# Optimization experiments

Hardware: AMD Instinct MI355X
Metric: run time of the kernel (lower is better)

The kernel has to match this reference:

```python
import jax, jax.numpy as jnp
import numpy as np

BS, M, D_IN, D_OUT = 32, 128, 64, 32


def _spd_log(X):
    # torch.svd on an SPD matrix == eigh (u diag(s) u^T with s>0), so
    # u @ diag(log s) @ v^T reduces to u @ diag(log s) @ u^T.
    s, u = jnp.linalg.eigh(X)
    return jnp.einsum('...ik,...k,...jk->...ij', u, jnp.log(s), u)


def _sym_exp(X):
    s, u = jnp.linalg.eigh(X)
    return jnp.einsum('...ik,...k,...jk->...ij', u, jnp.exp(s), u)


def setup_inputs() -> dict:
    key = jax.random.key(0)
    kx, kq, kk, kv = jax.random.split(key, 4)
    A = jax.random.normal(kx, (BS, M, D_IN, D_IN), dtype=jnp.float32)
    # SPD input: A A^T / d_in + eps I (eigenvalues strictly positive)
    x = jnp.einsum('bmij,bmkj->bmik', A, A) / D_IN + 1e-2 * jnp.eye(D_IN, dtype=jnp.float32)
    def stiefel(k):
        # column-orthonormal (d_in, d_out), mimicking SPDTransform's Stiefel weight
        return jnp.linalg.qr(jax.random.normal(k, (D_IN, D_OUT), dtype=jnp.float32))[0]
    return {'x': x, 'Wq': stiefel(kq), 'Wk': stiefel(kk), 'Wv': stiefel(kv)}


def reference(x, Wq, Wk, Wv):
    bs, m, d_in, _ = x.shape
    d_out = Wq.shape[1]

    def bimap(W):  # SPDTransform: W^T X W, stays SPD
        return jnp.einsum('pi,bmpq,qj->bmij', W, x, W)

    Q, K, V = bimap(Wq), bimap(Wk), bimap(Wv)
    logQ, logK, logV = _spd_log(Q), _spd_log(K), _spd_log(V)

    # log-Euclidean distance: sum of singular values of D D^T with
    # D = log A - log B (symmetric) equals trace(D D^T) = ||D||_F^2.
    # Torch's repeat/expand pattern yields energy[b,i,j] = d(K_i, Q_j);
    # computed here without materializing the (bs, m, m, d, d) tensor.
    q2 = jnp.sum(logQ * logQ, axis=(-2, -1))            # [bs, m]
    k2 = jnp.sum(logK * logK, axis=(-2, -1))            # [bs, m]
    cross = jnp.einsum('bikl,bjkl->bij', logK, logQ)    # [bs, m(i=K), m(j=Q)]
    energy = k2[:, :, None] + q2[:, None, :] - 2.0 * cross

    scores = 1.0 / (1.0 + jnp.log1p(energy))
    # softmax over dim=-2 (the K index i), then permute(0, 2, 1)
    attn = jnp.swapaxes(jax.nn.softmax(scores, axis=-2), -1, -2)  # [bs, j, i]

    # LogEuclideanMean: exp_sym( sum_i attn[b,j,i] * log V[b,i] )
    mean_log = jnp.einsum('bji,bikl->bjkl', attn, logV)
    out = _sym_exp(mean_log)
    return out.reshape(bs * m, d_out, d_out)
```

## Files before the change

### kernel.cpp

```cpp
#include <hip/hip_runtime.h>
#include <math.h>

constexpr int kBS = 32, kM = 128, kNMAT = kBS * kM;
constexpr int kDIN = 64, kDOUT = 32, kMSZ = kDOUT * kDOUT;
constexpr int kNSweep = 5;

constexpr size_t OFF_SS   = (size_t)3 * kNMAT * kMSZ;
constexpr size_t OFF_ATTN = OFF_SS + (size_t)3 * kNMAT;

#define F4(p)  (*(float4*)(p))
#define CF4(p) (*(const float4*)(p))

__global__ __launch_bounds__(256) void k_bimap(
    const float* __restrict__ x, const float* __restrict__ Wq,
    const float* __restrict__ Wk, const float* __restrict__ Wv,
    float* __restrict__ P) {
  __shared__ float Xs[64 * 68];
  __shared__ float Wsh[64 * 32];
  __shared__ float Ts[64 * 36];
  const int t = threadIdx.x;
  const int bm = blockIdx.x;
  const float* xp = x + (size_t)bm * (kDIN * kDIN);
  {
    const int f0 = t * 16;
    const int r = f0 >> 6, c = f0 & 63;
    const float* src = xp + f0;
    float* dst = &Xs[r * 68 + c];
#pragma unroll
    for (int i = 0; i < 4; ++i) F4(dst + 4 * i) = CF4(src + 4 * i);
  }
  const int r0 = (t >> 3) * 2;
  const int j0 = (t & 7) * 4;
  const int i2 = t >> 3;
  for (int tt = 0; tt < 3; ++tt) {
    const float* W = (tt == 0) ? Wq : ((tt == 1) ? Wk : Wv);
    __syncthreads();
    F4(&Wsh[t * 8]) = CF4(W + t * 8);
    F4(&Wsh[t * 8 + 4]) = CF4(W + t * 8 + 4);
    __syncthreads();
    float a0[4] = {0.f, 0.f, 0.f, 0.f}, a1[4] = {0.f, 0.f, 0.f, 0.f};
    for (int k = 0; k < 64; ++k) {
      const float2 x01 = *(const float2*)&Xs[k * 68 + r0];
      const float4 w = CF4(&Wsh[k * 32 + j0]);
      a0[0] += x01.x * w.x; a0[1] += x01.x * w.y; a0[2] += x01.x * w.z; a0[3] += x01.x * w.w;
      a1[0] += x01.y * w.x; a1[1] += x01.y * w.y; a1[2] += x01.y * w.z; a1[3] += x01.y * w.w;
    }
    F4(&Ts[r0 * 36 + j0])       = make_float4(a0[0], a0[1], a0[2], a0[3]);
    F4(&Ts[(r0 + 1) * 36 + j0]) = make_float4(a1[0], a1[1], a1[2], a1[3]);
    __syncthreads();
    float b4[4] = {0.f, 0.f, 0.f, 0.f};
    for (int p = 0; p < 64; ++p) {
      const float wv = Wsh[p * 32 + i2];
      const float4 tv = CF4(&Ts[p * 36 + j0]);
      b4[0] += wv * tv.x; b4[1] += wv * tv.y; b4[2] += wv * tv.z; b4[3] += wv * tv.w;
    }
    F4(&P[((size_t)tt * kNMAT + bm) * kMSZ + i2 * 32 + j0]) =
        make_float4(b4[0], b4[1], b4[2], b4[3]);
  }
}

constexpr int kJSlot = 32 * 36 + 32;
constexpr int kShl1 = 0x101, kShr1 = 0x111;

template <int CTRL>
__device__ __forceinline__ float updppf(float old_, float x) {
  return __builtin_bit_cast(float,
      __builtin_amdgcn_update_dpp(__builtin_bit_cast(int, old_),
                                  __builtin_bit_cast(int, x),
                                  CTRL, 0xf, 0xf, false));
}

__device__ __forceinline__ float xsign(float x, float s) {
  return __builtin_bit_cast(float,
      __builtin_bit_cast(int, x) ^
      (__builtin_bit_cast(int, s) & 0x80000000));
}

__global__ __launch_bounds__(256, 1) void k_jacobi_log(float* __restrict__ P,
                                                       float* __restrict__ sq) {
  __shared__ float lds[4 * kJSlot];
  const int t = threadIdx.x;
  const int wid = t >> 6, lane = t & 63;
  const int g = lane & 15;
  const int grp = lane >> 4;

  const bool is_g0 = (g == 0);
  const int p0 = is_g0 ? 31 : g;
  const int q0 = is_g0 ? 0 : 31 - g;

  const size_t gbase = (size_t)blockIdx.x * 16 + wid * 4;
  const float* A = P + (gbase + grp) * kMSZ;

  float cp[32], cq[32];
  {
    const float* pr = A + p0 * 32;
    const float* qr = A + q0 * 32;
#pragma unroll
    for (int i = 0; i < 32; i += 4) {
      const float4 a = CF4(pr + i);
      cp[i] = a.x; cp[i + 1] = a.y; cp[i + 2] = a.z; cp[i + 3] = a.w;
      const float4 b = CF4(qr + i);
      cq[i] = b.x; cq[i + 1] = b.y; cq[i + 2] = b.z; cq[i + 3] = b.w;
    }
  }
  float app, aqq;
  {
    float p0a = cp[0]*cp[0], p1a = cp[1]*cp[1];
    float q0a = cq[0]*cq[0], q1a = cq[1]*cq[1];
#pragma unroll
    for (int i = 2; i < 32; i += 2) {
      p0a = fmaf(cp[i], cp[i], p0a);  p1a = fmaf(cp[i+1], cp[i+1], p1a);
      q0a = fmaf(cq[i], cq[i], q0a);  q1a = fmaf(cq[i+1], cq[i+1], q1a);
    }
    app = p0a + p1a;
    aqq = q0a + q1a;
  }

  for (int sw = 0; sw < kNSweep; ++sw) {
    for (int r = 0; r < 31; ++r) {
      float d0 = cp[0]*cq[0], d1 = cp[1]*cq[1], d2 = cp[2]*cq[2], d3 = cp[3]*cq[3];
#pragma unroll
      for (int i = 4; i < 32; i += 4) {
        d0 = fmaf(cp[i],     cq[i],     d0);
        d1 = fmaf(cp[i + 1], cq[i + 1], d1);
        d2 = fmaf(cp[i + 2], cq[i + 2], d2);
        d3 = fmaf(cp[i + 3], cq[i + 3], d3);
      }
      const float apq = (d0 + d1) + (d2 + d3);
      const float d = aqq - app;
      const float apq2 = 2.f * apq;
      float h2 = fmaf(d, d, apq2 * apq2);
      h2 = fmaxf(h2, 1e-38f);
      const float hr = __builtin_amdgcn_rsqf(h2);
      const float h = h2 * hr;
      const float den = fabsf(d) + h;
      const float t0 = apq2 * __builtin_amdgcn_rcpf(den);
      const float tt = xsign(t0, d);
      const float c = __builtin_amdgcn_rsqf(fmaf(tt, tt, 1.f));
      const float sn = tt * c;
#pragma unroll
      for (int i = 0; i < 32; ++i) {
        const float np = fmaf(-sn, cq[i], c * cp[i]);
        const float nq = fmaf(c, cq[i], sn * cp[i]);
        const float cpm = updppf<kShl1>(nq, np);
        cp[i] = is_g0 ? np : cpm;
        cq[i] = updppf<kShr1>(cpm, nq);
      }
      const float c2 = c * c, s2 = sn * sn, cs2 = 2.f * c * sn;
      const float capp = fmaf(c2, app, fmaf(s2, aqq, -cs2 * apq));
      const float caqq = (app + aqq) - capp;
      const float capm = updppf<kShl1>(caqq, capp);
      app = is_g0 ? capp : capm;
      aqq = updppf<kShr1>(capm, caqq);
    }
  }
  float ssp, ssq;
  {
    float p0a = cp[0]*cp[0], p1a = cp[1]*cp[1];
    float q0a = cq[0]*cq[0], q1a = cq[1]*cq[1];
#pragma unroll
    for (int i = 2; i < 32; i += 2) {
      p0a = fmaf(cp[i], cp[i], p0a);  p1a = fmaf(cp[i+1], cp[i+1], p1a);
      q0a = fmaf(cq[i], cq[i], q0a);  q1a = fmaf(cq[i+1], cq[i+1], q1a);
    }
    ssp = p0a + p1a;
    ssq = q0a + q1a;
  }
  const float lgp = 0.5f * logf(ssp);
  const float lgq = 0.5f * logf(ssq);
  const float wp = lgp * __builtin_amdgcn_rcpf(ssp);
  const float wq = lgq * __builtin_amdgcn_rcpf(ssq);
  {
    float tot = fmaf(lgp, lgp, lgq * lgq);
    tot += __shfl_xor(tot, 1); tot += __shfl_xor(tot, 2);
    tot += __shfl_xor(tot, 4); tot += __shfl_xor(tot, 8);
    if (g == 0) sq[gbase + grp] = tot;
  }
  float* Bs = lds + wid * kJSlot;
  float* ncol = Bs + 1152;
  for (int m = 0; m < 4; ++m) {
    __builtin_amdgcn_wave_barrier();
    if (grp == m) {
#pragma unroll
      for (int i = 0; i < 32; i += 4) {
        F4(&Bs[p0 * 36 + i]) = make_float4(cp[i], cp[i+1], cp[i+2], cp[i+3]);
        F4(&Bs[q0 * 36 + i]) = make_float4(cq[i], cq[i+1], cq[i+2], cq[i+3]);
      }
      ncol[p0] = wp;
      ncol[q0] = wq;
    }
    __builtin_amdgcn_wave_barrier();
    {
      float* Am = P + (gbase + m) * kMSZ;
      const int rr = (lane >> 3) * 4, cc = (lane & 7) * 4;
      float acc[4][4] = {};
      for (int c = 0; c < 32; ++c) {
        const float w = ncol[c];
        const float4 br = CF4(&Bs[c * 36 + rr]);
        const float4 bc = CF4(&Bs[c * 36 + cc]);
        const float wr[4]  = {w * br.x, w * br.y, w * br.z, w * br.w};
        const float bcv[4] = {bc.x, bc.y, bc.z, bc.w};
#pragma unroll
        for (int i = 0; i < 4; ++i)
#pragma unroll
          for (int j2 = 0; j2 < 4; ++j2) acc[i][j2] += wr[i] * bcv[j2];
      }
#pragma unroll
      for (int i = 0; i < 4; ++i)
        F4(&Am[(rr + i) * 32 + cc]) =
            make_float4(acc[i][0], acc[i][1], acc[i][2], acc[i][3]);
    }
    __builtin_amdgcn_wave_barrier();
  }
}

__global__ __launch_bounds__(256) void k_attn(
    const float* __restrict__ P, const float* __restrict__ sq,
    float* __restrict__ attn) {
  __shared__ float Kt[32 * 132];
  __shared__ float Qt[32 * 20];
  __shared__ float Ss[128 * 20];
  __shared__ float red[16 * 20];
  __shared__ float mcol[16];
  __shared__ float scol[16];
  const int t = threadIdx.x;
  const int b = blockIdx.y, jt = blockIdx.x;
  const int j0g = jt * 16;
  const float* logK = P + ((size_t)kNMAT + (size_t)b * kM) * kMSZ;
  const float* logQ = P + ((size_t)b * kM + j0g) * kMSZ;
  const int i0 = (t >> 3) * 4, j0 = (t & 7) * 2;
  float acc[4][2] = {};
  for (int dc = 0; dc < kMSZ; dc += 32) {
    __syncthreads();
    {
      const int r = t >> 1, c0 = (t & 1) * 16;
      const float* src = logK + (size_t)r * kMSZ + dc + c0;
#pragma unroll
      for (int ii = 0; ii < 16; ii += 4) {
        const float4 v = CF4(src + ii);
        Kt[(c0 + ii + 0) * 132 + r] = v.x;
        Kt[(c0 + ii + 1) * 132 + r] = v.y;
        Kt[(c0 + ii + 2) * 132 + r] = v.z;
        Kt[(c0 + ii + 3) * 132 + r] = v.w;
      }
    }
    {
      const int j = t >> 4, c0 = (t & 15) * 2;
      const float2 v = *(const float2*)(logQ + (size_t)j * kMSZ + dc + c0);
      Qt[(c0 + 0) * 20 + j] = v.x;
      Qt[(c0 + 1) * 20 + j] = v.y;
    }
    __syncthreads();
    for (int k = 0; k < 32; ++k) {
      const float4 kv = CF4(&Kt[k * 132 + i0]);
      const float2 qv = *(const float2*)&Qt[k * 20 + j0];
      acc[0][0] = fmaf(kv.x, qv.x, acc[0][0]);
      acc[0][1] = fmaf(kv.x, qv.y, acc[0][1]);
      acc[1][0] = fmaf(kv.y, qv.x, acc[1][0]);
      acc[1][1] = fmaf(kv.y, qv.y, acc[1][1]);
      acc[2][0] = fmaf(kv.z, qv.x, acc[2][0]);
      acc[2][1] = fmaf(kv.z, qv.y, acc[2][1]);
      acc[3][0] = fmaf(kv.w, qv.x, acc[3][0]);
      acc[3][1] = fmaf(kv.w, qv.y, acc[3][1]);
    }
  }
  {
    float k2v[4], q2v[2];
#pragma unroll
    for (int i = 0; i < 4; ++i) k2v[i] = sq[kNMAT + b * kM + i0 + i];
#pragma unroll
    for (int j2 = 0; j2 < 2; ++j2) q2v[j2] = sq[b * kM + j0g + j0 + j2];
#pragma unroll
    for (int i = 0; i < 4; ++i)
#pragma unroll
      for (int j2 = 0; j2 < 2; ++j2) {
        float e = k2v[i] + q2v[j2] - 2.f * acc[i][j2];
        e = fmaxf(e, 0.f);
        Ss[(i0 + i) * 20 + (j0 + j2)] = 1.f / (1.f + log1pf(e));
      }
  }
  __syncthreads();
  const int jl = t & 15, grp = t >> 4;
  {
    float m = -1e30f;
#pragma unroll
    for (int i = 0; i < 8; ++i) m = fmaxf(m, Ss[(grp * 8 + i) * 20 + jl]);
    red[grp * 20 + jl] = m;
  }
  __syncthreads();
  if (t < 16) {
    float m = red[t];
#pragma unroll
    for (int g = 1; g < 16; ++g) m = fmaxf(m, red[g * 20 + t]);
    mcol[t] = m;
  }
  __syncthreads();
  {
    const float mj = mcol[jl];
    float s = 0.f;
#pragma unroll
    for (int i = 0; i < 8; ++i) s += expf(Ss[(grp * 8 + i) * 20 + jl] - mj);
    red[grp * 20 + jl] = s;
  }
  __syncthreads();
  if (t < 16) {
    float s = red[t];
#pragma unroll
    for (int g = 1; g < 16; ++g) s += red[g * 20 + t];
    scol[t] = 1.f / s;
  }
  __syncthreads();
  {
    const int il = t & 31, jg = t >> 5;
#pragma unroll
    for (int rep = 0; rep < 2; ++rep) {
      const int j2 = jg + rep * 8;
      const float mj = mcol[j2], is = scol[j2];
      float* dst = attn + ((size_t)b * kM + j0g + j2) * kM;
#pragma unroll
      for (int c4 = 0; c4 < 4; ++c4) {
        const int i = il + c4 * 32;
        dst[i] = expf(Ss[i * 20 + j2] - mj) * is;
      }
    }
  }
}

__global__ __launch_bounds__(256) void k_meanlog(
    const float* __restrict__ attn, const float* __restrict__ P,
    float* __restrict__ ML) {
  __shared__ float As[16 * 132];
  const int t = threadIdx.x;
  const int b = blockIdx.y, jt = blockIdx.x;
  const int j0g = jt * 16;
  const float* logV = P + ((size_t)2 * kNMAT + (size_t)b * kM) * kMSZ;
  {
    const int j = t >> 4, k0 = (t & 15) * 8;
    const float* src = attn + ((size_t)b * kM + j0g + j) * kM + k0;
    F4(&As[j * 132 + k0])     = CF4(src);
    F4(&As[j * 132 + k0 + 4]) = CF4(src + 4);
  }
  __syncthreads();
  const int d0 = t * 4;
  float acc[16][4] = {};
  for (int k = 0; k < kM; k += 4) {
    float4 vr[4];
#pragma unroll
    for (int kk = 0; kk < 4; ++kk)
      vr[kk] = CF4(&logV[(size_t)(k + kk) * kMSZ + d0]);
#pragma unroll
    for (int j = 0; j < 16; ++j) {
      const float4 w = CF4(&As[j * 132 + k]);
      const float wv[4] = {w.x, w.y, w.z, w.w};
#pragma unroll
      for (int kk = 0; kk < 4; ++kk) {
        const float* vv = (const float*)&vr[kk];
#pragma unroll
        for (int dd = 0; dd < 4; ++dd)
          acc[j][dd] = fmaf(wv[kk], vv[dd], acc[j][dd]);
      }
    }
  }
#pragma unroll
  for (int j = 0; j < 16; ++j)
    F4(&ML[((size_t)b * kM + j0g + j) * kMSZ + d0]) =
        make_float4(acc[j][0], acc[j][1], acc[j][2], acc[j][3]);
}

constexpr int kESlot = 2 * 1152;

__global__ __launch_bounds__(256) void k_expm(const float* __restrict__ ML,
                                              float* __restrict__ out) {
  __shared__ float lds[4 * kESlot];
  const int t = threadIdx.x;
  const int wid = t >> 6, lane = t & 63;
  const size_t bm = (size_t)blockIdx.x * 4 + wid;
  float* Mb = lds + wid * kESlot;
  float* Tb = Mb + 1152;
  const float* S = ML + bm * kMSZ;
  const int r = lane >> 1, c0 = (lane & 1) * 16;
  float4 v0 = CF4(S + r * 32 + c0),     v1 = CF4(S + r * 32 + c0 + 4),
         v2 = CF4(S + r * 32 + c0 + 8), v3 = CF4(S + r * 32 + c0 + 12);
  float lsum = v0.x*v0.x + v0.y*v0.y + v0.z*v0.z + v0.w*v0.w
             + v1.x*v1.x + v1.y*v1.y + v1.z*v1.z + v1.w*v1.w
             + v2.x*v2.x + v2.y*v2.y + v2.z*v2.z + v2.w*v2.w
             + v3.x*v3.x + v3.y*v3.y + v3.z*v3.z + v3.w*v3.w;
#pragma unroll
  for (int d = 1; d < 64; d <<= 1) lsum += __shfl_xor(lsum, d);
  const float fn = sqrtf(lsum);
  int sc = 0;
  if (fn > 0.5f) sc = (int)ceilf(log2f(fn * 2.0f));
  const float scale = exp2f((float)(-sc));
  v0.x*=scale; v0.y*=scale; v0.z*=scale; v0.w*=scale;
  v1.x*=scale; v1.y*=scale; v1.z*=scale; v1.w*=scale;
  v2.x*=scale; v2.y*=scale; v2.z*=scale; v2.w*=scale;
  v3.x*=scale; v3.y*=scale; v3.z*=scale; v3.w*=scale;
  F4(&Mb[r * 36 + c0])      = v0;
  F4(&Mb[r * 36 + c0 + 4])  = v1;
  F4(&Mb[r * 36 + c0 + 8])  = v2;
  F4(&Mb[r * 36 + c0 + 12]) = v3;
  __builtin_amdgcn_wave_barrier();
  const int rr = (lane >> 3) * 4, cc = (lane & 7) * 4;
#pragma unroll
  for (int i = 0; i < 4; ++i) {
    float4 v = F4(&Mb[(rr + i) * 36 + cc]);
    v.x = v.x * (1.f/7.f) + ((rr + i == cc + 0) ? 1.f : 0.f);
    v.y = v.y * (1.f/7.f) + ((rr + i == cc + 1) ? 1.f : 0.f);
    v.z = v.z * (1.f/7.f) + ((rr + i == cc + 2) ? 1.f : 0.f);
    v.w = v.w * (1.f/7.f) + ((rr + i == cc + 3) ? 1.f : 0.f);
    F4(&Tb[(rr + i) * 36 + cc]) = v;
  }
  __builtin_amdgcn_wave_barrier();
  for (int j = 6; j >= 1; --j) {
    float a4[4][4] = {};
    for (int k = 0; k < 32; ++k) {
      const float4 mv = CF4(&Mb[k * 36 + rr]);
      const float mvv[4] = {mv.x, mv.y, mv.z, mv.w};
      const float4 tv = CF4(&Tb[k * 36 + cc]);
      const float tvv[4] = {tv.x, tv.y, tv.z, tv.w};
#pragma unroll
      for (int i = 0; i < 4; ++i)
#pragma unroll
        for (int j2 = 0; j2 < 4; ++j2) a4[i][j2] += mvv[i] * tvv[j2];
    }
    const float inv = 1.f / (float)j;
#pragma unroll
    for (int i = 0; i < 4; ++i) {
      float4 v;
      v.x = a4[i][0] * inv + ((rr + i == cc + 0) ? 1.f : 0.f);
      v.y = a4[i][1] * inv + ((rr + i == cc + 1) ? 1.f : 0.f);
      v.z = a4[i][2] * inv + ((rr + i == cc + 2) ? 1.f : 0.f);
      v.w = a4[i][3] * inv + ((rr + i == cc + 3) ? 1.f : 0.f);
      F4(&Tb[(rr + i) * 36 + cc]) = v;
    }
    __builtin_amdgcn_wave_barrier();
  }
  for (int st = 0; st < sc; ++st) {
    float a4[4][4] = {};
    for (int k = 0; k < 32; ++k) {
      const float4 mv = CF4(&Tb[k * 36 + rr]);
      const float mvv[4] = {mv.x, mv.y, mv.z, mv.w};
      const float4 tv = CF4(&Tb[k * 36 + cc]);
      const float tvv[4] = {tv.x, tv.y, tv.z, tv.w};
#pragma unroll
      for (int i = 0; i < 4; ++i)
#pragma unroll
        for (int j2 = 0; j2 < 4; ++j2) a4[i][j2] += mvv[i] * tvv[j2];
    }
#pragma unroll
    for (int i = 0; i < 4; ++i)
      F4(&Tb[(rr + i) * 36 + cc]) =
          make_float4(a4[i][0], a4[i][1], a4[i][2], a4[i][3]);
    __builtin_amdgcn_wave_barrier();
  }
#pragma unroll
  for (int i = 0; i < 4; ++i) {
    const float4 v = CF4(&Tb[(rr + i) * 36 + cc]);
    F4(&out[bm * kMSZ + (rr + i) * 32 + cc]) = v;
  }
}

extern "C" void kernel_launch(void* const* d_in, const int* in_sizes, int n_in,
                              void* d_out, int out_size, void* d_ws, size_t ws_size,
                              hipStream_t stream) {
  const float* x  = (const float*)d_in[0];
  const float* Wq = (const float*)d_in[1];
  const float* Wk = (const float*)d_in[2];
  const float* Wv = (const float*)d_in[3];
  float* ws   = (float*)d_ws;
  float* P    = ws;
  float* sq   = ws + OFF_SS;
  float* attn = ws + OFF_ATTN;
  float* ML   = ws;
  float* out  = (float*)d_out;

  k_bimap<<<kNMAT, 256, 0, stream>>>(x, Wq, Wk, Wv, P);
  k_jacobi_log<<<3 * kNMAT / 16, 256, 0, stream>>>(P, sq);
  k_attn<<<dim3(8, kBS), 256, 0, stream>>>(P, sq, attn);
  k_meanlog<<<dim3(8, kBS), 256, 0, stream>>>(attn, P, ML);
  k_expm<<<kNMAT / 4, 256, 0, stream>>>(ML, out);
}
```

Baseline: 480.6 us.

## Split Jacobi eigensolver rows across two half-groups to halve per-thread registers

```diff
diff --git a/kernel.cpp b/kernel.cpp
--- a/kernel.cpp
+++ b/kernel.cpp
@@ -76,57 +76,70 @@
       (__builtin_bit_cast(int, s) & 0x80000000));
 }
 
-__global__ __launch_bounds__(256, 1) void k_jacobi_log(float* __restrict__ P,
+__global__ __launch_bounds__(256, 6) void k_jacobi_log(float* __restrict__ P,
                                                        float* __restrict__ sq) {
   __shared__ float lds[4 * kJSlot];
   const int t = threadIdx.x;
   const int wid = t >> 6, lane = t & 63;
+  const int mat = lane >> 5;
   const int g = lane & 15;
-  const int grp = lane >> 4;
+  const int sub = (lane >> 4) & 1;
+  const int off = sub * 16;
 
   const bool is_g0 = (g == 0);
+  const bool is_g15 = (g == 15);
   const int p0 = is_g0 ? 31 : g;
   const int q0 = is_g0 ? 0 : 31 - g;
 
-  const size_t gbase = (size_t)blockIdx.x * 16 + wid * 4;
-  const float* A = P + (gbase + grp) * kMSZ;
-
-  float cp[32], cq[32];
-  {
-    const float* pr = A + p0 * 32;
-    const float* qr = A + q0 * 32;
-#pragma unroll
-    for (int i = 0; i < 32; i += 4) {
+  const size_t gbase = (size_t)blockIdx.x * 8 + wid * 2;
+  const float* A = P + (gbase + mat) * kMSZ;
+
+  float2 cp2[8], cq2[8];
+  {
+    const float* pr = A + p0 * 32 + off;
+    const float* qr = A + q0 * 32 + off;
+#pragma unroll
+    for (int i = 0; i < 16; i += 4) {
       const float4 a = CF4(pr + i);
-      cp[i] = a.x; cp[i + 1] = a.y; cp[i + 2] = a.z; cp[i + 3] = a.w;
+      cp2[i / 2]     = make_float2(a.x, a.y);
+      cp2[i / 2 + 1] = make_float2(a.z, a.w);
       const float4 b = CF4(qr + i);
-      cq[i] = b.x; cq[i + 1] = b.y; cq[i + 2] = b.z; cq[i + 3] = b.w;
+      cq2[i / 2]     = make_float2(b.x, b.y);
+      cq2[i / 2 + 1] = make_float2(b.z, b.w);
     }
   }
   float app, aqq;
   {
-    float p0a = cp[0]*cp[0], p1a = cp[1]*cp[1];
-    float q0a = cq[0]*cq[0], q1a = cq[1]*cq[1];
-#pragma unroll
-    for (int i = 2; i < 32; i += 2) {
-      p0a = fmaf(cp[i], cp[i], p0a);  p1a = fmaf(cp[i+1], cp[i+1], p1a);
-      q0a = fmaf(cq[i], cq[i], q0a);  q1a = fmaf(cq[i+1], cq[i+1], q1a);
-    }
-    app = p0a + p1a;
-    aqq = q0a + q1a;
-  }
+    float2 pa, qa;
+    pa.x = cp2[0].x * cp2[0].x;  pa.y = cp2[0].y * cp2[0].y;
+    qa.x = cq2[0].x * cq2[0].x;  qa.y = cq2[0].y * cq2[0].y;
+#pragma unroll
+    for (int j = 1; j < 8; ++j) {
+      pa.x = fmaf(cp2[j].x, cp2[j].x, pa.x);
+      pa.y = fmaf(cp2[j].y, cp2[j].y, pa.y);
+      qa.x = fmaf(cq2[j].x, cq2[j].x, qa.x);
+      qa.y = fmaf(cq2[j].y, cq2[j].y, qa.y);
+    }
+    app = pa.x + pa.y;
+    aqq = qa.x + qa.y;
+  }
+  app += __shfl_xor(app, 16);
+  aqq += __shfl_xor(aqq, 16);
 
   for (int sw = 0; sw < kNSweep; ++sw) {
     for (int r = 0; r < 31; ++r) {
-      float d0 = cp[0]*cq[0], d1 = cp[1]*cq[1], d2 = cp[2]*cq[2], d3 = cp[3]*cq[3];
-#pragma unroll
-      for (int i = 4; i < 32; i += 4) {
-        d0 = fmaf(cp[i],     cq[i],     d0);
-        d1 = fmaf(cp[i + 1], cq[i + 1], d1);
-        d2 = fmaf(cp[i + 2], cq[i + 2], d2);
-        d3 = fmaf(cp[i + 3], cq[i + 3], d3);
-      }
-      const float apq = (d0 + d1) + (d2 + d3);
+      float2 dA, dB;
+      dA.x = cp2[0].x * cq2[0].x;  dA.y = cp2[0].y * cq2[0].y;
+      dB.x = cp2[1].x * cq2[1].x;  dB.y = cp2[1].y * cq2[1].y;
+#pragma unroll
+      for (int j = 2; j < 8; j += 2) {
+        dA.x = fmaf(cp2[j].x, cq2[j].x, dA.x);
+        dA.y = fmaf(cp2[j].y, cq2[j].y, dA.y);
+        dB.x = fmaf(cp2[j + 1].x, cq2[j + 1].x, dB.x);
+        dB.y = fmaf(cp2[j + 1].y, cq2[j + 1].y, dB.y);
+      }
+      float apq = (dA.x + dA.y) + (dB.x + dB.y);
+      apq += __shfl_xor(apq, 16);
       const float d = aqq - app;
       const float apq2 = 2.f * apq;
       float h2 = fmaf(d, d, apq2 * apq2);
@@ -139,33 +152,52 @@
       const float c = __builtin_amdgcn_rsqf(fmaf(tt, tt, 1.f));
       const float sn = tt * c;
 #pragma unroll
-      for (int i = 0; i < 32; ++i) {
-        const float np = fmaf(-sn, cq[i], c * cp[i]);
-        const float nq = fmaf(c, cq[i], sn * cp[i]);
-        const float cpm = updppf<kShl1>(nq, np);
-        cp[i] = is_g0 ? np : cpm;
-        cq[i] = updppf<kShr1>(cpm, nq);
+      for (int j = 0; j < 8; ++j) {
+        {
+          const float cpc = cp2[j].x, cqc = cq2[j].x;
+          const float np_ = fmaf(-sn, cqc, c * cpc);
+          const float nq_ = fmaf(c, cqc, sn * cpc);
+          float tv = is_g15 ? nq_ : cqc;
+          tv = updppf<kShl1>(tv, np_);
+          cp2[j].x = is_g0 ? np_ : tv;
+          cq2[j].x = updppf<kShr1>(tv, nq_);
+        }
+        {
+          const float cpc = cp2[j].y, cqc = cq2[j].y;
+          const float np_ = fmaf(-sn, cqc, c * cpc);
+          const float nq_ = fmaf(c, cqc, sn * cpc);
+          float tv = is_g15 ? nq_ : cqc;
+          tv = updppf<kShl1>(tv, np_);
+          cp2[j].y = is_g0 ? np_ : tv;
+          cq2[j].y = updppf<kShr1>(tv, nq_);
+        }
       }
       const float c2 = c * c, s2 = sn * sn, cs2 = 2.f * c * sn;
       const float capp = fmaf(c2, app, fmaf(s2, aqq, -cs2 * apq));
       const float caqq = (app + aqq) - capp;
-      const float capm = updppf<kShl1>(caqq, capp);
-      app = is_g0 ? capp : capm;
-      aqq = updppf<kShr1>(capm, caqq);
+      float tn = is_g15 ? caqq : app;
+      tn = updppf<kShl1>(tn, capp);
+      app = is_g0 ? capp : tn;
+      aqq = updppf<kShr1>(tn, caqq);
     }
   }
   float ssp, ssq;
   {
-    float p0a = cp[0]*cp[0], p1a = cp[1]*cp[1];
-    float q0a = cq[0]*cq[0], q1a = cq[1]*cq[1];
-#pragma unroll
-    for (int i = 2; i < 32; i += 2) {
-      p0a = fmaf(cp[i], cp[i], p0a);  p1a = fmaf(cp[i+1], cp[i+1], p1a);
-      q0a = fmaf(cq[i], cq[i], q0a);  q1a = fmaf(cq[i+1], cq[i+1], q1a);
-    }
-    ssp = p0a + p1a;
-    ssq = q0a + q1a;
-  }
+    float2 pa, qa;
+    pa.x = cp2[0].x * cp2[0].x;  pa.y = cp2[0].y * cp2[0].y;
+    qa.x = cq2[0].x * cq2[0].x;  qa.y = cq2[0].y * cq2[0].y;
+#pragma unroll
+    for (int j = 1; j < 8; ++j) {
+      pa.x = fmaf(cp2[j].x, cp2[j].x, pa.x);
+      pa.y = fmaf(cp2[j].y, cp2[j].y, pa.y);
+      qa.x = fmaf(cq2[j].x, cq2[j].x, qa.x);
+      qa.y = fmaf(cq2[j].y, cq2[j].y, qa.y);
+    }
+    ssp = pa.x + pa.y;
+    ssq = qa.x + qa.y;
+  }
+  ssp += __shfl_xor(ssp, 16);
+  ssq += __shfl_xor(ssq, 16);
   const float lgp = 0.5f * logf(ssp);
   const float lgq = 0.5f * logf(ssq);
   const float wp = lgp * __builtin_amdgcn_rcpf(ssp);
@@ -174,20 +206,24 @@
     float tot = fmaf(lgp, lgp, lgq * lgq);
     tot += __shfl_xor(tot, 1); tot += __shfl_xor(tot, 2);
     tot += __shfl_xor(tot, 4); tot += __shfl_xor(tot, 8);
-    if (g == 0) sq[gbase + grp] = tot;
+    if ((lane & 31) == 0) sq[gbase + mat] = tot;
   }
   float* Bs = lds + wid * kJSlot;
   float* ncol = Bs + 1152;
-  for (int m = 0; m < 4; ++m) {
+  for (int m = 0; m < 2; ++m) {
     __builtin_amdgcn_wave_barrier();
-    if (grp == m) {
-#pragma unroll
-      for (int i = 0; i < 32; i += 4) {
-        F4(&Bs[p0 * 36 + i]) = make_float4(cp[i], cp[i+1], cp[i+2], cp[i+3]);
-        F4(&Bs[q0 * 36 + i]) = make_float4(cq[i], cq[i+1], cq[i+2], cq[i+3]);
-      }
-      ncol[p0] = wp;
-      ncol[q0] = wq;
+    if (mat == m) {
+#pragma unroll
+      for (int i = 0; i < 16; i += 4) {
+        F4(&Bs[p0 * 36 + off + i]) = make_float4(cp2[i/2].x, cp2[i/2].y,
+                                                 cp2[i/2+1].x, cp2[i/2+1].y);
+        F4(&Bs[q0 * 36 + off + i]) = make_float4(cq2[i/2].x, cq2[i/2].y,
+                                                 cq2[i/2+1].x, cq2[i/2+1].y);
+      }
+      if (sub == 0) {
+        ncol[p0] = wp;
+        ncol[q0] = wq;
+      }
     }
     __builtin_amdgcn_wave_barrier();
     {
@@ -475,7 +511,7 @@
   float* out  = (float*)d_out;
 
   k_bimap<<<kNMAT, 256, 0, stream>>>(x, Wq, Wk, Wv, P);
-  k_jacobi_log<<<3 * kNMAT / 16, 256, 0, stream>>>(P, sq);
+  k_jacobi_log<<<3 * kNMAT / 8, 256, 0, stream>>>(P, sq);
   k_attn<<<dim3(8, kBS), 256, 0, stream>>>(P, sq, attn);
   k_meanlog<<<dim3(8, kBS), 256, 0, stream>>>(attn, P, ML);
   k_expm<<<kNMAT / 4, 256, 0, stream>>>(ML, out);
```

Measured after the change: 556.3 us. +15.8%, slower.
